# Optimization experiments

Hardware: AMD Instinct MI355X
Metric: run time of the kernel (lower is better)

Reference implementation:

```python
import jax, jax.numpy as jnp
import numpy as np

NUM_VIEWS = 6
NUM_HEADS = 16
NUM_LAYERS = 2
DIST_THRESHOLD = 10.0
EPS = 1e-5


def layer_norm(x, g, b):
    m = jnp.mean(x, axis=-1, keepdims=True)
    v = jnp.mean((x - m) ** 2, axis=-1, keepdims=True)
    return (x - m) / jnp.sqrt(v + EPS) * g + b


def build_mask(coords3d, num_views, threshold):
    # coords3d: (B, T, 3) -> bool mask (B, T, T), True = masked
    B, T, _ = coords3d.shape
    tpv = T // num_views
    c = jnp.nan_to_num(coords3d, nan=0.0, posinf=100.0, neginf=-100.0)
    view_ids = jnp.repeat(jnp.arange(num_views), tpv)
    same_view = view_ids[:, None] == view_ids[None, :]  # (T, T)
    dist_sq = jnp.sum((c[:, :, None, :] - c[:, None, :, :]) ** 2, axis=-1)  # (B,T,T)
    mask = same_view[None] | (dist_sq > threshold * threshold)
    all_masked = jnp.all(mask, axis=-1)  # (B, T)
    eye = jnp.eye(T, dtype=bool)
    # unmask diagonal for rows that are fully masked (matches torch fix)
    mask = jnp.where(all_masked[:, :, None] & eye[None], False, mask)
    return mask


def mha(x, qkv_w, qkv_b, out_w, out_b, mask, num_heads):
    # x: (B,T,C); qkv_w: (3C,C); out_w: (C,C); mask: (B,T,T) True=masked
    B, T, C = x.shape
    hd = C // num_heads
    qkv = x @ qkv_w.T + qkv_b  # (B,T,3C)
    q, k, v = jnp.split(qkv, 3, axis=-1)
    def heads(t):
        return t.reshape(B, T, num_heads, hd).transpose(0, 2, 1, 3)  # (B,H,T,hd)
    q, k, v = heads(q), heads(k), heads(v)
    scale = 1.0 / jnp.sqrt(jnp.asarray(hd, x.dtype))
    scores = jnp.einsum('bhqd,bhkd->bhqk', q * scale, k)
    scores = jnp.where(mask[:, None], -jnp.inf, scores)
    attn = jax.nn.softmax(scores, axis=-1)
    o = jnp.einsum('bhqk,bhkd->bhqd', attn, v)  # (B,H,T,hd)
    o = o.transpose(0, 2, 1, 3).reshape(B, T, C)
    return o @ out_w.T + out_b


def setup_inputs() -> dict:
    key = jax.random.key(0)
    B, T, C, L = 2, 1536, 1024, NUM_LAYERS
    ks = jax.random.split(key, 16)
    s = 0.02
    inp = {
        'pos_embed': jax.random.normal(ks[0], (B, T, C), jnp.float32),
        'coords3d': jax.random.normal(ks[1], (B, T, 3), jnp.float32) * 8.0,
        'ln1_g': jnp.ones((L, C), jnp.float32),
        'ln1_b': jnp.zeros((L, C), jnp.float32),
        'qkv_w': jax.random.normal(ks[2], (L, 3 * C, C), jnp.float32) * s,
        'qkv_b': jnp.zeros((L, 3 * C), jnp.float32),
        'out_w': jax.random.normal(ks[3], (L, C, C), jnp.float32) * s,
        'out_b': jnp.zeros((L, C), jnp.float32),
        'ln2_g': jnp.ones((L, C), jnp.float32),
        'ln2_b': jnp.zeros((L, C), jnp.float32),
        'ffn_w1': jax.random.normal(ks[4], (L, 4 * C, C), jnp.float32) * s,
        'ffn_b1': jnp.zeros((L, 4 * C), jnp.float32),
        'ffn_w2': jax.random.normal(ks[5], (L, C, 4 * C), jnp.float32) * s,
        'ffn_b2': jnp.zeros((L, C), jnp.float32),
        'norm_g': jnp.ones((C,), jnp.float32),
        'norm_b': jnp.zeros((C,), jnp.float32),
    }
    return inp


def reference(pos_embed, coords3d, ln1_g, ln1_b, qkv_w, qkv_b, out_w, out_b,
              ln2_g, ln2_b, ffn_w1, ffn_b1, ffn_w2, ffn_b2, norm_g, norm_b):
    mask = build_mask(coords3d, NUM_VIEWS, DIST_THRESHOLD)
    x = pos_embed
    for l in range(NUM_LAYERS):
        xn = layer_norm(x, ln1_g[l], ln1_b[l])
        x = x + mha(xn, qkv_w[l], qkv_b[l], out_w[l], out_b[l], mask, NUM_HEADS)
        xn = layer_norm(x, ln2_g[l], ln2_b[l])
        h = jax.nn.gelu(xn @ ffn_w1[l].T + ffn_b1[l], approximate=False)
        x = x + (h @ ffn_w2[l].T + ffn_b2[l])
    return layer_norm(x, norm_g, norm_b)
```

## Files before the change

### kernel.cpp

```cpp
#include <hip/hip_runtime.h>

#define TT 1536
#define CC 1024
#define NH 16
#define HD 64
#define NL 2
#define NB 2
#define MM (NB*TT)

typedef unsigned short u16;
typedef unsigned int u32;
typedef unsigned long long u64;
typedef __attribute__((ext_vector_type(8))) short short8v;
typedef __attribute__((ext_vector_type(4))) float f32x4;

__device__ __forceinline__ u16 f2bf(float f){
  u32 u = __float_as_uint(f);
  u32 r = (u + 0x7FFFu + ((u >> 16) & 1u)) >> 16;
  return (u16)r;
}

__device__ __forceinline__ void gload_lds16(const void* g, void* l){
  __builtin_amdgcn_global_load_lds(
      (const __attribute__((address_space(1))) void*)g,
      (__attribute__((address_space(3))) void*)l, 16, 0, 0);
}

__device__ __forceinline__ f32x4 mfma16(short8v a, short8v b, f32x4 c){
  return __builtin_amdgcn_mfma_f32_16x16x32_bf16(a, b, c, 0, 0, 0);
}

__device__ __forceinline__ float exp2f_fast(float x){
  return __builtin_amdgcn_exp2f(x);
}

__device__ __forceinline__ u32 cvt_pk_bf16(float lo, float hi){
  u32 r;
  asm("v_cvt_pk_bf16_f32 %0, %1, %2" : "=v"(r) : "v"(lo), "v"(hi));
  return r;
}

__device__ __forceinline__ char* ldsw(void* base, int row, int colb){
  return (char*)base + row * 128 + (colb ^ ((row & 7) << 4));
}

__global__ __launch_bounds__(256) void cvt_bf16_kernel(const float* __restrict__ in,
                                                       u16* __restrict__ out, int n4){
  int stride = gridDim.x * 256;
  for (int i = blockIdx.x * 256 + threadIdx.x; i < n4; i += stride){
    const float4 v = ((const float4*)in)[i];
    ushort4 o;
    o.x = f2bf(v.x); o.y = f2bf(v.y); o.z = f2bf(v.z); o.w = f2bf(v.w);
    ((ushort4*)out)[i] = o;
  }
}

__device__ __forceinline__ float fixc(float v){
  if (__builtin_isnan(v)) return 0.0f;
  if (__builtin_isinf(v)) return v > 0.0f ? 100.0f : -100.0f;
  return v;
}

__global__ __launch_bounds__(256) void mask_kernel(const float* __restrict__ coords,
                                                   u64* __restrict__ maskw){
  const int tid = threadIdx.x, wave = tid >> 6, lane = tid & 63;
  const int ri = blockIdx.x * 4 + wave;
  const int b = ri / TT, i = ri - b * TT;
  const float* cp = coords + (size_t)ri * 3;
  const float cx = fixc(cp[0]), cy = fixc(cp[1]), cz = fixc(cp[2]);
  const int vi = i >> 8;
  u64 allm = ~0ull;
  for (int ch = 0; ch < 24; ++ch){
    const int j = ch * 64 + lane;
    const float* cj = coords + ((size_t)b * TT + j) * 3;
    const float dx = cx - fixc(cj[0]);
    const float dy = cy - fixc(cj[1]);
    const float dz = cz - fixc(cj[2]);
    const float d2 = dx*dx + dy*dy + dz*dz;
    const bool masked = ((j >> 8) == vi) || (d2 > 100.0f);
    const u64 bal = __ballot(masked);
    if (lane == 0) maskw[(size_t)ri * 24 + ch] = bal;
    allm &= bal;
  }
  if (lane == 0 && allm == ~0ull){
    const size_t w = (size_t)ri * 24 + (i >> 6);
    maskw[w] &= ~(1ull << (i & 63));
  }
}

template<int OUTF>
__global__ __launch_bounds__(256) void ln_kernel(const float* __restrict__ x,
    const float* __restrict__ gw, const float* __restrict__ bw,
    u16* __restrict__ outb, float* __restrict__ outf){
  __shared__ float sred[4];
  const int tid = threadIdx.x, wave = tid >> 6, lane = tid & 63;
  const size_t row = blockIdx.x;
  const float4 v = *(const float4*)(x + row * CC + tid * 4);
  float s = v.x + v.y + v.z + v.w;
  #pragma unroll
  for (int o = 1; o < 64; o <<= 1) s += __shfl_xor(s, o, 64);
  if (lane == 0) sred[wave] = s;
  __syncthreads();
  const float mean = (sred[0] + sred[1] + sred[2] + sred[3]) * (1.0f / CC);
  __syncthreads();
  const float d0 = v.x - mean, d1 = v.y - mean, d2 = v.z - mean, d3 = v.w - mean;
  float q = d0*d0 + d1*d1 + d2*d2 + d3*d3;
  #pragma unroll
  for (int o = 1; o < 64; o <<= 1) q += __shfl_xor(q, o, 64);
  if (lane == 0) sred[wave] = q;
  __syncthreads();
  const float var = (sred[0] + sred[1] + sred[2] + sred[3]) * (1.0f / CC);
  const float rstd = rsqrtf(var + 1e-5f);
  const float4 g4 = *(const float4*)(gw + tid * 4);
  const float4 b4 = *(const float4*)(bw + tid * 4);
  const float y0 = d0 * rstd * g4.x + b4.x;
  const float y1 = d1 * rstd * g4.y + b4.y;
  const float y2 = d2 * rstd * g4.z + b4.z;
  const float y3 = d3 * rstd * g4.w + b4.w;
  if (OUTF){
    *(float4*)(outf + row * CC + tid * 4) = make_float4(y0, y1, y2, y3);
  } else {
    ushort4 o4; o4.x = f2bf(y0); o4.y = f2bf(y1); o4.z = f2bf(y2); o4.w = f2bf(y3);
    *(ushort4*)(outb + row * CC + tid * 4) = o4;
  }
}

template<int EPI>
__global__ __launch_bounds__(512, 4) void gemm_nt(const u16* __restrict__ A,
    const u16* __restrict__ Bw, const float* __restrict__ bias,
    const float* __restrict__ res, u16* __restrict__ outb, float* __restrict__ outf,
    int M, int N, int K){
  __shared__ u16 As[2][128][64];
  __shared__ u16 Bs[2][128][64];
  const int tid = threadIdx.x, wave = tid >> 6, lane = tid & 63;
  const int gx = gridDim.x;
  const int nwg = gx * gridDim.y;
  const int orig = blockIdx.y * gx + blockIdx.x;
  const int qq = nwg >> 3, rm = nwg & 7;
  const int xcd = orig & 7, pos = orig >> 3;
  const int wg = (xcd < rm ? xcd * (qq + 1) : rm * (qq + 1) + (xcd - rm) * qq) + pos;
  const int m0 = (wg / gx) * 128, n0 = (wg % gx) * 128;
  const int wr = wave >> 1, wc = wave & 1;
  f32x4 acc[2][4];
  #pragma unroll
  for (int mi = 0; mi < 2; ++mi)
    #pragma unroll
    for (int ni = 0; ni < 4; ++ni){ f32x4 z = {0.f,0.f,0.f,0.f}; acc[mi][ni] = z; }

  const u16* Ag = A + (size_t)m0 * K;
  const u16* Bg = Bw + (size_t)n0 * K;
  const int srow0 = wave * 8 + (lane >> 3);
  const int scole = ((lane & 7) ^ (lane >> 3)) * 8;
  auto stage = [&](int buf, int k0){
    char* ab = (char*)&As[buf][0][0];
    char* bb = (char*)&Bs[buf][0][0];
    #pragma unroll
    for (int l = 0; l < 2; ++l){
      const size_t goff = (size_t)(l*64 + srow0) * K + k0 + scole;
      const int loff = (l*8 + wave) * 1024;
      gload_lds16(Ag + goff, ab + loff);
      gload_lds16(Bg + goff, bb + loff);
    }
  };

  const int NT = K >> 6;
  stage(0, 0);
  stage(1, 64);

  const int ar = lane & 15, akb = (lane >> 4) * 16;
  const int rsw = (ar & 7) << 4;
  for (int t = 0; t < NT; ++t){
    const int cur = t & 1;
    if (t + 1 < NT) asm volatile("s_waitcnt vmcnt(4)" ::: "memory");
    else            asm volatile("s_waitcnt vmcnt(0)" ::: "memory");
    __builtin_amdgcn_s_barrier();
    const char* ab = (const char*)&As[cur][0][0];
    const char* bb = (const char*)&Bs[cur][0][0];
    short8v af[2][2], bf[4][2];
    #pragma unroll
    for (int ks = 0; ks < 2; ++ks){
      const int cb = (ks*64 + akb) ^ rsw;
      #pragma unroll
      for (int mi = 0; mi < 2; ++mi)
        af[mi][ks] = *(const short8v*)(ab + (wr*32 + mi*16 + ar)*128 + cb);
      #pragma unroll
      for (int ni = 0; ni < 4; ++ni)
        bf[ni][ks] = *(const short8v*)(bb + (wc*64 + ni*16 + ar)*128 + cb);
    }
    asm volatile("s_waitcnt lgkmcnt(0)" ::: "memory");
    __builtin_amdgcn_sched_barrier(0);
    __builtin_amdgcn_s_barrier();
    if (t + 2 < NT) stage(cur, (t + 2) * 64);
    __builtin_amdgcn_s_setprio(1);
    #pragma unroll
    for (int ks = 0; ks < 2; ++ks)
      #pragma unroll
      for (int mi = 0; mi < 2; ++mi)
        #pragma unroll
        for (int ni = 0; ni < 4; ++ni)
          acc[mi][ni] = mfma16(af[mi][ks], bf[ni][ks], acc[mi][ni]);
    __builtin_amdgcn_s_setprio(0);
  }

  const int cr = (lane >> 4) * 4, cl = lane & 15;
  #pragma unroll
  for (int ni = 0; ni < 4; ++ni){
    const int c = n0 + wc*64 + ni*16 + cl;
    const float bv = bias[c];
    #pragma unroll
    for (int mi = 0; mi < 2; ++mi){
      #pragma unroll
      for (int r = 0; r < 4; ++r){
        const size_t rr2 = (size_t)(m0 + wr*32 + mi*16 + cr + r);
        float v = acc[mi][ni][r] + bv;
        if constexpr (EPI == 1) v = 0.5f * v * (1.0f + erff(v * 0.70710678118654752f));
        if constexpr (EPI == 2) outf[rr2 * N + c] = v + res[rr2 * N + c];
        else outb[rr2 * N + c] = f2bf(v);
      }
    }
  }
}

__global__ __launch_bounds__(256) void attn_kernel(const u16* __restrict__ qkv,
    const u64* __restrict__ maskw, u16* __restrict__ outp){
  __shared__ u16 Ks[2][64][64];
  __shared__ u16 Vt[2][64][64];
  __shared__ u16 Ps[4][16][64];
  const int tid = threadIdx.x, wave = tid >> 6, lane = tid & 63;
  const int b = blockIdx.y >> 4, h = blockIdx.y & 15;
  const int qb = blockIdx.x * 64;
  const int rs = 3 * CC;
  const int g4 = lane >> 4;
  const int l15 = lane & 15;
  const int qrow = qb + wave * 16 + l15;

  const float qscale = 0.18033688011112042f;
  const u16* qp = qkv + (size_t)(b * TT + qrow) * rs + h * HD + g4 * 8;
  short8v qf0, qf1;
  {
    const short8v r0 = *(const short8v*)qp;
    const short8v r1 = *(const short8v*)(qp + 32);
    #pragma unroll
    for (int e = 0; e < 8; ++e){
      qf0[e] = (short)f2bf(__uint_as_float(((u32)(u16)r0[e]) << 16) * qscale);
      qf1[e] = (short)f2bf(__uint_as_float(((u32)(u16)r1[e]) << 16) * qscale);
    }
  }

  f32x4 o[4], lacc;
  #pragma unroll
  for (int dt = 0; dt < 4; ++dt){ f32x4 z = {0.f,0.f,0.f,0.f}; o[dt] = z; }
  { f32x4 z = {0.f,0.f,0.f,0.f}; lacc = z; }
  float m_r = -1.0e4f;

  u16* psb = &Ps[wave][0][0];
  const u64* mrow_p = maskw + (size_t)(b * TT + qrow) * 24;

  short8v vone;
  #pragma unroll
  for (int e = 0; e < 8; ++e) vone[e] = (short)0x3F80;

  auto stageK = [&](int t, int buf){
    const int j0 = t * 64;
    #pragma unroll
    for (int l = 0; l < 2; ++l){
      const int off = (wave * 2 + l) * 1024;
      const int krow = (off >> 7) + (lane >> 3);
      const int kcolb = ((lane & 7) * 16) ^ ((krow & 7) << 4);
      gload_lds16(qkv + (size_t)(b * TT + j0 + krow) * rs + CC + h * HD + (kcolb >> 1),
                  (char*)(&Ks[buf][0][0]) + off);
    }
  };
  u16 vv[16];
  auto loadV = [&](int t){
    const int j0 = t * 64;
    #pragma unroll
    for (int it = 0; it < 2; ++it){
      const int jc = it * 4 + wave;
      #pragma unroll
      for (int e = 0; e < 8; ++e)
        vv[it*8+e] = qkv[(size_t)(b * TT + j0 + jc * 8 + e) * rs + 2 * CC + h * HD + lane];
    }
  };
  auto writeV = [&](int buf){
    #pragma unroll
    for (int it = 0; it < 2; ++it){
      const int jc = it * 4 + wave;
      short8v sv;
      #pragma unroll
      for (int e = 0; e < 8; ++e) sv[e] = (short)vv[it*8+e];
      *(short8v*)ldsw(&Vt[buf][0][0], lane, jc * 16) = sv;
    }
  };

  loadV(0);
  stageK(0, 0);
  writeV(0);
  __syncthreads();

  for (int t = 0; t < TT / 64; ++t){
    const int cur = t & 1;
    const bool pf = (t < TT / 64 - 1);
    if (pf){ loadV(t + 1); stageK(t + 1, cur ^ 1); }

    const u64 mw = mrow_p[t];
    const u32 mwlo = (u32)mw, mwhi = (u32)(mw >> 32);

    const char* Kc = (const char*)&Ks[cur][0][0];
    f32x4 S[4];
    #pragma unroll
    for (int jt = 0; jt < 4; ++jt){
      const short8v k0 = *(const short8v*)ldsw((void*)Kc, jt*16 + l15, g4 * 16);
      const short8v k1 = *(const short8v*)ldsw((void*)Kc, jt*16 + l15, 64 + g4 * 16);
      f32x4 z = {0.f,0.f,0.f,0.f};
      z = mfma16(k0, qf0, z);
      z = mfma16(k1, qf1, z);
      S[jt] = z;
    }

    float ps[16];
    float cmax = -3.0e38f;
    #pragma unroll
    for (int jt = 0; jt < 4; ++jt){
      const u32 msrc = (jt & 2) ? mwhi : mwlo;
      const int sh = g4 * 4 + (jt & 1) * 16;
      #pragma unroll
      for (int r = 0; r < 4; ++r){
        float s = S[jt][r];
        s = ((msrc >> (sh + r)) & 1u) ? -3.0e38f : s;
        ps[jt*4+r] = s;
        cmax = fmaxf(cmax, s);
      }
    }
    cmax = fmaxf(cmax, __shfl_xor(cmax, 16));
    cmax = fmaxf(cmax, __shfl_xor(cmax, 32));

    if (!__all(cmax <= m_r + 8.0f)){
      const float mnew = fmaxf(m_r, cmax);
      const float fac = exp2f_fast(m_r - mnew);
      m_r = mnew;
      float fr4[4];
      #pragma unroll
      for (int r = 0; r < 4; ++r) fr4[r] = __shfl(fac, g4 * 4 + r);
      #pragma unroll
      for (int dt = 0; dt < 4; ++dt){
        f32x4 tt = o[dt];
        tt[0] *= fr4[0]; tt[1] *= fr4[1]; tt[2] *= fr4[2]; tt[3] *= fr4[3];
        o[dt] = tt;
      }
      lacc[0] *= fr4[0]; lacc[1] *= fr4[1]; lacc[2] *= fr4[2]; lacc[3] *= fr4[3];
    }

    #pragma unroll
    for (int i = 0; i < 16; ++i) ps[i] = exp2f_fast(ps[i] - m_r);

    #pragma unroll
    for (int jt = 0; jt < 4; ++jt){
      uint2 pk;
      pk.x = cvt_pk_bf16(ps[jt*4+0], ps[jt*4+1]);
      pk.y = cvt_pk_bf16(ps[jt*4+2], ps[jt*4+3]);
      *(uint2*)ldsw(psb, l15, jt * 32 + g4 * 8) = pk;
    }

    short8v pA[2];
    #pragma unroll
    for (int kc = 0; kc < 2; ++kc)
      pA[kc] = *(const short8v*)ldsw(psb, l15, kc * 64 + g4 * 16);
    char* Vc = (char*)&Vt[cur][0][0];
    #pragma unroll
    for (int dt = 0; dt < 4; ++dt){
      #pragma unroll
      for (int kc = 0; kc < 2; ++kc){
        const short8v vf = *(const short8v*)ldsw(Vc, dt*16 + l15, kc * 64 + g4 * 16);
        o[dt] = mfma16(pA[kc], vf, o[dt]);
      }
    }
    lacc = mfma16(pA[0], vone, lacc);
    lacc = mfma16(pA[1], vone, lacc);

    if (pf) writeV(cur ^ 1);
    __syncthreads();
  }

  float linv[4];
  #pragma unroll
  for (int r = 0; r < 4; ++r) linv[r] = 1.0f / fmaxf(lacc[r], 1e-30f);
  #pragma unroll
  for (int dt = 0; dt < 4; ++dt)
    #pragma unroll
    for (int r = 0; r < 4; ++r)
      outp[(size_t)(b * TT + qb + wave * 16 + g4 * 4 + r) * CC + h * HD + dt * 16 + l15] =
          f2bf(o[dt][r] * linv[r]);
}

extern "C" void kernel_launch(void* const* d_in, const int* in_sizes, int n_in,
                              void* d_out, int out_size, void* d_ws, size_t ws_size,
                              hipStream_t stream){
  (void)in_sizes; (void)n_in; (void)out_size; (void)ws_size;
  const float* pos    = (const float*)d_in[0];
  const float* coords = (const float*)d_in[1];
  const float* ln1g   = (const float*)d_in[2];
  const float* ln1b   = (const float*)d_in[3];
  const float* qkvw   = (const float*)d_in[4];
  const float* qkvbi  = (const float*)d_in[5];
  const float* outw   = (const float*)d_in[6];
  const float* outbi  = (const float*)d_in[7];
  const float* ln2g   = (const float*)d_in[8];
  const float* ln2b   = (const float*)d_in[9];
  const float* w1     = (const float*)d_in[10];
  const float* b1     = (const float*)d_in[11];
  const float* w2     = (const float*)d_in[12];
  const float* b2     = (const float*)d_in[13];
  const float* ng     = (const float*)d_in[14];
  const float* nbb    = (const float*)d_in[15];

  char* wsp = (char*)d_ws;
  size_t off = 0;
  auto alloc = [&](size_t bytes)->void*{
    void* p = wsp + off; off += (bytes + 255) & ~(size_t)255; return p;
  };
  u16* qkvw_bf = (u16*)alloc((size_t)NL*3*CC*CC*sizeof(u16));
  u16* outw_bf = (u16*)alloc((size_t)NL*CC*CC*sizeof(u16));
  u16* w1_bf   = (u16*)alloc((size_t)NL*4*CC*CC*sizeof(u16));
  u16* w2_bf   = (u16*)alloc((size_t)NL*4*CC*CC*sizeof(u16));
  float* x     = (float*)alloc((size_t)MM*CC*sizeof(float));
  u16* xn      = (u16*)alloc((size_t)MM*CC*sizeof(u16));
  u16* qkvbuf  = (u16*)alloc((size_t)MM*4*CC*sizeof(u16));
  u16* attnb   = (u16*)alloc((size_t)MM*CC*sizeof(u16));
  u64* maskw   = (u64*)alloc((size_t)MM*24*sizeof(u64));
  u16* hbuf = qkvbuf;

  auto cvt = [&](const float* s, u16* dst, size_t n){
    int n4 = (int)(n >> 2);
    int blocks = (n4 + 255) / 256; if (blocks > 4096) blocks = 4096;
    cvt_bf16_kernel<<<dim3(blocks), dim3(256), 0, stream>>>(s, dst, n4);
  };
  cvt(qkvw, qkvw_bf, (size_t)NL*3*CC*CC);
  cvt(outw, outw_bf, (size_t)NL*CC*CC);
  cvt(w1, w1_bf, (size_t)NL*4*CC*CC);
  cvt(w2, w2_bf, (size_t)NL*4*CC*CC);

  hipMemcpyAsync(x, pos, (size_t)MM*CC*sizeof(float), hipMemcpyDeviceToDevice, stream);
  mask_kernel<<<dim3(MM/4), dim3(256), 0, stream>>>(coords, maskw);

  for (int l = 0; l < NL; ++l){
    ln_kernel<0><<<dim3(MM), dim3(256), 0, stream>>>(x, ln1g + l*CC, ln1b + l*CC, xn, nullptr);
    gemm_nt<0><<<dim3(3*CC/128, MM/128), dim3(512), 0, stream>>>(
        xn, qkvw_bf + (size_t)l*3*CC*CC, qkvbi + l*3*CC, nullptr, qkvbuf, nullptr, MM, 3*CC, CC);
    attn_kernel<<<dim3(TT/64, NB*NH), dim3(256), 0, stream>>>(qkvbuf, maskw, attnb);
    gemm_nt<2><<<dim3(CC/128, MM/128), dim3(512), 0, stream>>>(
        attnb, outw_bf + (size_t)l*CC*CC, outbi + l*CC, x, nullptr, x, MM, CC, CC);
    ln_kernel<0><<<dim3(MM), dim3(256), 0, stream>>>(x, ln2g + l*CC, ln2b + l*CC, xn, nullptr);
    gemm_nt<1><<<dim3(4*CC/128, MM/128), dim3(512), 0, stream>>>(
        xn, w1_bf + (size_t)l*4*CC*CC, b1 + l*4*CC, nullptr, hbuf, nullptr, MM, 4*CC, CC);
    gemm_nt<2><<<dim3(CC/128, MM/128), dim3(512), 0, stream>>>(
        hbuf, w2_bf + (size_t)l*4*CC*CC, b2 + l*CC, x, nullptr, x, MM, CC, 4*CC);
  }
  ln_kernel<1><<<dim3(MM), dim3(256), 0, stream>>>(x, ng, nbb, nullptr, (float*)d_out);
}
```

Before: 461.4 us.

## Split-K with atomic residual accumulation for narrow GEMMs; restructure attention loop

The out-projection and FFN-down GEMMs (N=1024, only 192 tiles) now use split-K across blockIdx.z (2 and 4 slices). Each slice atomically adds its partial product into the fp32 residual buffer, with the bias added only by slice 0. This replaces the separate residual read and raises the number of workgroups to fill the GPU. The attention kernel is also restructured: LDS offsets are precomputed, global pointers are incremented instead of recomputed, the loop is unrolled by two, MFMA priority is raised, and launch bounds are set to 3 blocks. Atomic fp32 adds make the summation order nondeterministic and add atomic traffic.

```diff
diff --git a/kernel.cpp b/kernel.cpp
--- a/kernel.cpp
+++ b/kernel.cpp
@@ -128,8 +128,8 @@
 template<int EPI>
 __global__ __launch_bounds__(512, 4) void gemm_nt(const u16* __restrict__ A,
     const u16* __restrict__ Bw, const float* __restrict__ bias,
-    const float* __restrict__ res, u16* __restrict__ outb, float* __restrict__ outf,
-    int M, int N, int K){
+    u16* __restrict__ outb, float* __restrict__ outf,
+    int M, int N, int K, int Ksl){
   __shared__ u16 As[2][128][64];
   __shared__ u16 Bs[2][128][64];
   const int tid = threadIdx.x, wave = tid >> 6, lane = tid & 63;
@@ -140,6 +140,7 @@
   const int xcd = orig & 7, pos = orig >> 3;
   const int wg = (xcd < rm ? xcd * (qq + 1) : rm * (qq + 1) + (xcd - rm) * qq) + pos;
   const int m0 = (wg / gx) * 128, n0 = (wg % gx) * 128;
+  const int kz = blockIdx.z;
   const int wr = wave >> 1, wc = wave & 1;
   f32x4 acc[2][4];
   #pragma unroll
@@ -147,8 +148,8 @@
     #pragma unroll
     for (int ni = 0; ni < 4; ++ni){ f32x4 z = {0.f,0.f,0.f,0.f}; acc[mi][ni] = z; }
 
-  const u16* Ag = A + (size_t)m0 * K;
-  const u16* Bg = Bw + (size_t)n0 * K;
+  const u16* Ag = A + (size_t)m0 * K + (size_t)kz * Ksl;
+  const u16* Bg = Bw + (size_t)n0 * K + (size_t)kz * Ksl;
   const int srow0 = wave * 8 + (lane >> 3);
   const int scole = ((lane & 7) ^ (lane >> 3)) * 8;
   auto stage = [&](int buf, int k0){
@@ -163,7 +164,7 @@
     }
   };
 
-  const int NT = K >> 6;
+  const int NT = Ksl >> 6;
   stage(0, 0);
   stage(1, 64);
 
@@ -212,16 +213,22 @@
       #pragma unroll
       for (int r = 0; r < 4; ++r){
         const size_t rr2 = (size_t)(m0 + wr*32 + mi*16 + cr + r);
-        float v = acc[mi][ni][r] + bv;
-        if constexpr (EPI == 1) v = 0.5f * v * (1.0f + erff(v * 0.70710678118654752f));
-        if constexpr (EPI == 2) outf[rr2 * N + c] = v + res[rr2 * N + c];
-        else outb[rr2 * N + c] = f2bf(v);
+        float v = acc[mi][ni][r];
+        if constexpr (EPI == 3){
+          v += (kz == 0) ? bv : 0.0f;
+          __hip_atomic_fetch_add(&outf[rr2 * N + c], v, __ATOMIC_RELAXED,
+                                 __HIP_MEMORY_SCOPE_AGENT);
+        } else {
+          v += bv;
+          if constexpr (EPI == 1) v = 0.5f * v * (1.0f + erff(v * 0.70710678118654752f));
+          outb[rr2 * N + c] = f2bf(v);
+        }
       }
     }
   }
 }
 
-__global__ __launch_bounds__(256) void attn_kernel(const u16* __restrict__ qkv,
+__global__ __launch_bounds__(256, 3) void attn_kernel(const u16* __restrict__ qkv,
     const u64* __restrict__ maskw, u16* __restrict__ outp){
   __shared__ u16 Ks[2][64][64];
   __shared__ u16 Vt[2][64][64];
@@ -233,9 +240,10 @@
   const int g4 = lane >> 4;
   const int l15 = lane & 15;
   const int qrow = qb + wave * 16 + l15;
+  const u16* kv_base = qkv + (size_t)b * TT * rs;
 
   const float qscale = 0.18033688011112042f;
-  const u16* qp = qkv + (size_t)(b * TT + qrow) * rs + h * HD + g4 * 8;
+  const u16* qp = kv_base + (size_t)qrow * rs + h * HD + g4 * 8;
   short8v qf0, qf1;
   {
     const short8v r0 = *(const short8v*)qp;
@@ -253,65 +261,75 @@
   { f32x4 z = {0.f,0.f,0.f,0.f}; lacc = z; }
   float m_r = -1.0e4f;
 
-  u16* psb = &Ps[wave][0][0];
-  const u64* mrow_p = maskw + (size_t)(b * TT + qrow) * 24;
+  const int sw = (l15 & 7) << 4;
+  const int swl = (lane & 7) << 4;
+  int koff[4][2], voff[4][2], pwoff[4], proff[2], vwoff[2];
+  #pragma unroll
+  for (int jt = 0; jt < 4; ++jt){
+    koff[jt][0] = (jt*16 + l15)*128 + ((g4*16) ^ sw);
+    koff[jt][1] = (jt*16 + l15)*128 + ((64 + g4*16) ^ sw);
+    voff[jt][0] = koff[jt][0];
+    voff[jt][1] = koff[jt][1];
+    pwoff[jt] = wave*2048 + l15*128 + ((jt*32 + g4*8) ^ sw);
+  }
+  proff[0] = wave*2048 + l15*128 + ((g4*16) ^ sw);
+  proff[1] = wave*2048 + l15*128 + ((64 + g4*16) ^ sw);
+  vwoff[0] = lane*128 + ((wave*16) ^ swl);
+  vwoff[1] = lane*128 + ((64 + wave*16) ^ swl);
+
+  const int scol = CC + h * HD + (((lane & 7) ^ (lane >> 3)) * 8);
+  const u16* skp0 = kv_base + (size_t)(64 + wave*16 + (lane >> 3)) * rs + scol;
+  const u16* skp1 = skp0 + 8 * rs;
+  const u16* vp   = kv_base + (size_t)(64 + wave*8) * rs + 2*CC + h*HD + lane;
+  const u64* mp2  = maskw + (size_t)(b * TT + qrow) * 24;
+
+  char* KsB = (char*)&Ks[0][0][0];
+  char* VtB = (char*)&Vt[0][0][0];
+  char* PsB = (char*)&Ps[0][0][0];
 
   short8v vone;
   #pragma unroll
   for (int e = 0; e < 8; ++e) vone[e] = (short)0x3F80;
 
-  auto stageK = [&](int t, int buf){
-    const int j0 = t * 64;
-    #pragma unroll
-    for (int l = 0; l < 2; ++l){
-      const int off = (wave * 2 + l) * 1024;
-      const int krow = (off >> 7) + (lane >> 3);
-      const int kcolb = ((lane & 7) * 16) ^ ((krow & 7) << 4);
-      gload_lds16(qkv + (size_t)(b * TT + j0 + krow) * rs + CC + h * HD + (kcolb >> 1),
-                  (char*)(&Ks[buf][0][0]) + off);
-    }
-  };
-  u16 vv[16];
-  auto loadV = [&](int t){
-    const int j0 = t * 64;
-    #pragma unroll
-    for (int it = 0; it < 2; ++it){
-      const int jc = it * 4 + wave;
-      #pragma unroll
-      for (int e = 0; e < 8; ++e)
-        vv[it*8+e] = qkv[(size_t)(b * TT + j0 + jc * 8 + e) * rs + 2 * CC + h * HD + lane];
-    }
-  };
-  auto writeV = [&](int buf){
-    #pragma unroll
-    for (int it = 0; it < 2; ++it){
-      const int jc = it * 4 + wave;
-      short8v sv;
-      #pragma unroll
-      for (int e = 0; e < 8; ++e) sv[e] = (short)vv[it*8+e];
-      *(short8v*)ldsw(&Vt[buf][0][0], lane, jc * 16) = sv;
-    }
-  };
-
-  loadV(0);
-  stageK(0, 0);
-  writeV(0);
-  __syncthreads();
-
-  for (int t = 0; t < TT / 64; ++t){
-    const int cur = t & 1;
-    const bool pf = (t < TT / 64 - 1);
-    if (pf){ loadV(t + 1); stageK(t + 1, cur ^ 1); }
-
-    const u64 mw = mrow_p[t];
+  {
+    u16 vv[16];
+    #pragma unroll
+    for (int e = 0; e < 8; ++e)
+      vv[e] = kv_base[(size_t)(wave*8 + e) * rs + 2*CC + h*HD + lane];
+    #pragma unroll
+    for (int e = 0; e < 8; ++e)
+      vv[8+e] = kv_base[(size_t)(32 + wave*8 + e) * rs + 2*CC + h*HD + lane];
+    gload_lds16(kv_base + (size_t)(wave*16 + (lane>>3)) * rs + scol,
+                KsB + (wave*2 + 0) * 1024);
+    gload_lds16(kv_base + (size_t)(wave*16 + 8 + (lane>>3)) * rs + scol,
+                KsB + (wave*2 + 1) * 1024);
+    short8v sv0, sv1;
+    #pragma unroll
+    for (int e = 0; e < 8; ++e){ sv0[e] = (short)vv[e]; sv1[e] = (short)vv[8+e]; }
+    *(short8v*)(VtB + vwoff[0]) = sv0;
+    *(short8v*)(VtB + vwoff[1]) = sv1;
+    __syncthreads();
+  }
+
+  auto chunk = [&](int buf, bool pf){
+    u16 vv[16];
+    if (pf){
+      #pragma unroll
+      for (int e = 0; e < 8; ++e) vv[e] = vp[(size_t)e * rs];
+      #pragma unroll
+      for (int e = 0; e < 8; ++e) vv[8+e] = vp[(size_t)(32 + e) * rs];
+      gload_lds16(skp0, KsB + (buf^1)*8192 + (wave*2 + 0)*1024);
+      gload_lds16(skp1, KsB + (buf^1)*8192 + (wave*2 + 1)*1024);
+    }
+    const u64 mw = mp2[buf];
     const u32 mwlo = (u32)mw, mwhi = (u32)(mw >> 32);
 
-    const char* Kc = (const char*)&Ks[cur][0][0];
+    const char* Kb = KsB + buf * 8192;
     f32x4 S[4];
     #pragma unroll
     for (int jt = 0; jt < 4; ++jt){
-      const short8v k0 = *(const short8v*)ldsw((void*)Kc, jt*16 + l15, g4 * 16);
-      const short8v k1 = *(const short8v*)ldsw((void*)Kc, jt*16 + l15, 64 + g4 * 16);
+      const short8v k0 = *(const short8v*)(Kb + koff[jt][0]);
+      const short8v k1 = *(const short8v*)(Kb + koff[jt][1]);
       f32x4 z = {0.f,0.f,0.f,0.f};
       z = mfma16(k0, qf0, z);
       z = mfma16(k1, qf1, z);
@@ -359,27 +377,42 @@
       uint2 pk;
       pk.x = cvt_pk_bf16(ps[jt*4+0], ps[jt*4+1]);
       pk.y = cvt_pk_bf16(ps[jt*4+2], ps[jt*4+3]);
-      *(uint2*)ldsw(psb, l15, jt * 32 + g4 * 8) = pk;
+      *(uint2*)(PsB + pwoff[jt]) = pk;
     }
 
     short8v pA[2];
-    #pragma unroll
-    for (int kc = 0; kc < 2; ++kc)
-      pA[kc] = *(const short8v*)ldsw(psb, l15, kc * 64 + g4 * 16);
-    char* Vc = (char*)&Vt[cur][0][0];
+    pA[0] = *(const short8v*)(PsB + proff[0]);
+    pA[1] = *(const short8v*)(PsB + proff[1]);
+    const char* Vb = VtB + buf * 8192;
+    __builtin_amdgcn_s_setprio(1);
     #pragma unroll
     for (int dt = 0; dt < 4; ++dt){
       #pragma unroll
       for (int kc = 0; kc < 2; ++kc){
-        const short8v vf = *(const short8v*)ldsw(Vc, dt*16 + l15, kc * 64 + g4 * 16);
+        const short8v vf = *(const short8v*)(Vb + voff[dt][kc]);
         o[dt] = mfma16(pA[kc], vf, o[dt]);
       }
     }
     lacc = mfma16(pA[0], vone, lacc);
     lacc = mfma16(pA[1], vone, lacc);
-
-    if (pf) writeV(cur ^ 1);
+    __builtin_amdgcn_s_setprio(0);
+
+    if (pf){
+      short8v sv0, sv1;
+      #pragma unroll
+      for (int e = 0; e < 8; ++e){ sv0[e] = (short)vv[e]; sv1[e] = (short)vv[8+e]; }
+      char* Vd = VtB + (buf^1) * 8192;
+      *(short8v*)(Vd + vwoff[0]) = sv0;
+      *(short8v*)(Vd + vwoff[1]) = sv1;
+      vp += (size_t)64 * rs; skp0 += (size_t)64 * rs; skp1 += (size_t)64 * rs;
+    }
     __syncthreads();
+  };
+
+  for (int th = 0; th < 12; ++th){
+    chunk(0, true);
+    chunk(1, th < 11);
+    mp2 += 2;
   }
 
   float linv[4];
@@ -445,16 +478,16 @@
 
   for (int l = 0; l < NL; ++l){
     ln_kernel<0><<<dim3(MM), dim3(256), 0, stream>>>(x, ln1g + l*CC, ln1b + l*CC, xn, nullptr);
-    gemm_nt<0><<<dim3(3*CC/128, MM/128), dim3(512), 0, stream>>>(
-        xn, qkvw_bf + (size_t)l*3*CC*CC, qkvbi + l*3*CC, nullptr, qkvbuf, nullptr, MM, 3*CC, CC);
+    gemm_nt<0><<<dim3(3*CC/128, MM/128, 1), dim3(512), 0, stream>>>(
+        xn, qkvw_bf + (size_t)l*3*CC*CC, qkvbi + l*3*CC, qkvbuf, nullptr, MM, 3*CC, CC, CC);
     attn_kernel<<<dim3(TT/64, NB*NH), dim3(256), 0, stream>>>(qkvbuf, maskw, attnb);
-    gemm_nt<2><<<dim3(CC/128, MM/128), dim3(512), 0, stream>>>(
-        attnb, outw_bf + (size_t)l*CC*CC, outbi + l*CC, x, nullptr, x, MM, CC, CC);
+    gemm_nt<3><<<dim3(CC/128, MM/128, 2), dim3(512), 0, stream>>>(
+        attnb, outw_bf + (size_t)l*CC*CC, outbi + l*CC, nullptr, x, MM, CC, CC, CC/2);
     ln_kernel<0><<<dim3(MM), dim3(256), 0, stream>>>(x, ln2g + l*CC, ln2b + l*CC, xn, nullptr);
-    gemm_nt<1><<<dim3(4*CC/128, MM/128), dim3(512), 0, stream>>>(
-        xn, w1_bf + (size_t)l*4*CC*CC, b1 + l*4*CC, nullptr, hbuf, nullptr, MM, 4*CC, CC);
-    gemm_nt<2><<<dim3(CC/128, MM/128), dim3(512), 0, stream>>>(
-        hbuf, w2_bf + (size_t)l*4*CC*CC, b2 + l*CC, x, nullptr, x, MM, CC, 4*CC);
+    gemm_nt<1><<<dim3(4*CC/128, MM/128, 1), dim3(512), 0, stream>>>(
+        xn, w1_bf + (size_t)l*4*CC*CC, b1 + l*4*CC, hbuf, nullptr, MM, 4*CC, CC, CC);
+    gemm_nt<3><<<dim3(CC/128, MM/128, 4), dim3(512), 0, stream>>>(
+        hbuf, w2_bf + (size_t)l*4*CC*CC, b2 + l*CC, nullptr, x, MM, CC, 4*CC, CC);
   }
   ln_kernel<1><<<dim3(MM), dim3(256), 0, stream>>>(x, ng, nbb, nullptr, (float*)d_out);
 }
```

Result: slower. 489.4 us (+6.1%).
